# Kernel optimization log

Measured on AMD Instinct MI355X. Metric: run time of the kernel, lower is better.

## Reference

```python
import math
import jax, jax.numpy as jnp
import numpy as np


def conv2d(x, w, stride=1, padding=0, groups=1):
    return jax.lax.conv_general_dilated(
        x, w, (stride, stride), [(padding, padding), (padding, padding)],
        feature_group_count=groups, dimension_numbers=('NCHW', 'OIHW', 'NCHW'))


def bn_relu(x, g, b, eps=1e-5):
    # training-mode batchnorm (batch statistics, biased var) + ReLU
    m = x.mean(axis=(0, 2, 3), keepdims=True)
    v = x.var(axis=(0, 2, 3), keepdims=True)
    y = (x - m) * jax.lax.rsqrt(v + eps)
    return jax.nn.relu(y * g[None, :, None, None] + b[None, :, None, None])


def up2x(x):
    B, C, H, W = x.shape
    return jax.image.resize(x, (B, C, 2 * H, 2 * W), 'bilinear')


def pos2d(C, H, W):
    # faithful port of ReasonDecoder.pos2d -> [H*W, 1, C]
    dm = C // 2
    div = jnp.exp(jnp.arange(0.0, dm, 2.0) * (-(math.log(10000.0) / dm)))  # [dm//2]
    pos_w = jnp.arange(0.0, W)[:, None]
    pos_h = jnp.arange(0.0, H)[:, None]
    sw = jnp.sin(pos_w * div).T  # [dm//2, W]
    cw = jnp.cos(pos_w * div).T
    sh = jnp.sin(pos_h * div).T  # [dm//2, H]
    ch = jnp.cos(pos_h * div).T
    pe = jnp.zeros((C, H, W))
    pe = pe.at[0:dm:2].set(jnp.broadcast_to(sw[:, None, :], (dm // 2, H, W)))
    pe = pe.at[1:dm:2].set(jnp.broadcast_to(cw[:, None, :], (dm // 2, H, W)))
    pe = pe.at[dm::2].set(jnp.broadcast_to(sh[:, :, None], (dm // 2, H, W)))
    pe = pe.at[dm + 1::2].set(jnp.broadcast_to(ch[:, :, None], (dm // 2, H, W)))
    return pe.reshape(C, 1, H * W).transpose(2, 1, 0)


def setup_inputs() -> dict:
    key = jax.random.key(0)
    ks = jax.random.split(key, 32)
    B, C, H, W = 8, 512, 32, 32
    Cv = 256  # in_dim of Projector
    KS = 3
    s = 0.02
    inp = {
        'image_embeddings': jax.random.normal(ks[0], (B, C, H, W), jnp.float32),
        'sparse_prompt_embeddings': jax.random.normal(ks[1], (B, 2, C), jnp.float32),
        'state': jax.random.normal(ks[2], (B, C), jnp.float32),
        'multimask_output': 0,
        # stand-in transformer: single linear on (src + pos)
        'W_t': jax.random.normal(ks[3], (C, C), jnp.float32) * s,
        'iou_token': jax.random.normal(ks[4], (1, C), jnp.float32) * s,
        'mask_tokens': jax.random.normal(ks[5], (4, C), jnp.float32) * s,
        # Projector.vis
        'vis_conv1_w': jax.random.normal(ks[6], (2 * Cv, 2 * Cv, 3, 3), jnp.float32) * s,
        'vis_bn1_g': jnp.ones((2 * Cv,), jnp.float32),
        'vis_bn1_b': jnp.zeros((2 * Cv,), jnp.float32),
        'vis_conv2_w': jax.random.normal(ks[7], (Cv, 2 * Cv, 3, 3), jnp.float32) * s,
        'vis_bn2_g': jnp.ones((Cv,), jnp.float32),
        'vis_bn2_b': jnp.zeros((Cv,), jnp.float32),
        'vis_conv3_w': jax.random.normal(ks[8], (Cv, Cv, 1, 1), jnp.float32) * s,
        'vis_conv3_b': jnp.zeros((Cv,), jnp.float32),
        # Projector.txt -> Linear(512, 256*3*3 + 1)
        'txt_w': jax.random.normal(ks[9], (Cv * KS * KS + 1, C), jnp.float32) * s,
        'txt_b': jnp.zeros((Cv * KS * KS + 1,), jnp.float32),
        # 1x1 convs as linears
        'ln_ans_w': jax.random.normal(ks[10], (512, 512), jnp.float32) * s,
        'ln_ans_b': jnp.zeros((512,), jnp.float32),
        'ln_ans2_w': jax.random.normal(ks[11], (128, 512), jnp.float32) * s,
        'ln_ans2_b': jnp.zeros((128,), jnp.float32),
        # router: Linear(1024,256) -> ReLU -> Linear(256,8)
        'router_w1': jax.random.normal(ks[12], (256, 1024), jnp.float32) * s,
        'router_b1': jnp.zeros((256,), jnp.float32),
        'router_w2': jax.random.normal(ks[13], (8, 256), jnp.float32) * s,
        'router_b2': jnp.zeros((8,), jnp.float32),
        # 8 experts: Linear(128, 23) each, stacked
        'experts_w': jax.random.normal(ks[14], (8, 23, 128), jnp.float32) * s,
        'experts_b': jnp.zeros((8, 23), jnp.float32),
    }
    return inp


def reference(image_embeddings, sparse_prompt_embeddings, state, multimask_output,
              W_t, iou_token, mask_tokens,
              vis_conv1_w, vis_bn1_g, vis_bn1_b,
              vis_conv2_w, vis_bn2_g, vis_bn2_b,
              vis_conv3_w, vis_conv3_b,
              txt_w, txt_b, ln_ans_w, ln_ans_b, ln_ans2_w, ln_ans2_b,
              router_w1, router_b1, router_w2, router_b2,
              experts_w, experts_b):
    B, C, H, W = image_embeddings.shape
    pe = pos2d(C, H, W)  # [HW,1,C]

    # tokens = [iou, mask tokens, sparse prompts] (passed to transformer; hs unused)
    out_tok = jnp.concatenate([iou_token, mask_tokens], axis=0)  # [5,C]
    tokens = jnp.concatenate(
        [jnp.broadcast_to(out_tok[None], (B,) + out_tok.shape), sparse_prompt_embeddings], axis=1)
    del tokens  # hs is discarded by predict_masks

    # stand-in transformer: src_out = Linear(src_flat + pos)
    src_flat = image_embeddings.reshape(B, C, H * W).transpose(0, 2, 1) + pe[:, 0, :][None]  # [B,HW,C]
    src_flat = jnp.einsum('bnc,dc->bnd', src_flat, W_t)
    src = src_flat.transpose(0, 2, 1).reshape(B, C, H, W)

    # ---- Projector ----
    ans = src.mean(axis=(2, 3))                              # global avg pool [B,512]
    ans_vec = ans @ ln_ans_w.T + ln_ans_b                    # 1x1 conv [B,512]

    x = up2x(src)
    x = bn_relu(conv2d(x, vis_conv1_w, padding=1), vis_bn1_g, vis_bn1_b)
    x = up2x(x)
    x = bn_relu(conv2d(x, vis_conv2_w, padding=1), vis_bn2_g, vis_bn2_b)
    x = conv2d(x, vis_conv3_w) + vis_conv3_b[None, :, None, None]  # [B,256,4H,4W]
    Bx, Cx, Hx, Wx = x.shape

    qa = jnp.concatenate([state, ans_vec], axis=1)           # [B,1024]
    o = jax.nn.softmax(qa, axis=1) * qa
    half = o.shape[1] // 2
    word = o[:, :half] + o[:, half:]                         # [B,512]
    word = word @ txt_w.T + txt_b                            # [B, 256*9+1]
    dyn_w = word[:, :-1].reshape(B, Cx, 3, 3)                # per-sample conv weights
    dyn_b = word[:, -1]                                      # [B]

    xg = x.reshape(1, B * Cx, Hx, Wx)
    out = conv2d(xg, dyn_w, padding=1, groups=B) + dyn_b[None, :, None, None]  # [1,B,Hx,Wx]
    masks = out.transpose(1, 0, 2, 3)                        # [B,1,Hx,Wx]

    gates = jax.nn.softmax(
        jax.nn.relu(qa @ router_w1.T + router_b1) @ router_w2.T + router_b2, axis=1)  # [B,8]
    feat128 = ans_vec @ ln_ans2_w.T + ln_ans2_b              # [B,128]
    logits = jnp.einsum('be,eof,bf->bo', gates, experts_w, feat128) + gates @ experts_b  # [B,23]

    masks = masks[:, 1:, :, :] if multimask_output else masks[:, 0:1, :, :]
    return masks, logits, src
```

## Files before the change

kernel.cpp:

```cpp
#include <hip/hip_runtime.h>
#include <hip/hip_bf16.h>

typedef __attribute__((ext_vector_type(8))) short short8;
typedef __attribute__((ext_vector_type(4))) short shortx4;
typedef __attribute__((ext_vector_type(4))) float floatx4;
typedef __attribute__((ext_vector_type(16))) float floatx16;

#define F2BF __float2bfloat16
#define BF2F __bfloat162float

#define WS_W4R2   0UL
#define WS_WRO2   9437184UL
#define WS_WRO1   11796480UL
#define WS_Y1     16515072UL
#define WS_Y2     50069504UL
#define WS_W4R1   50069504UL
#define WS_A      68943872UL
#define WS_WTB    77332480UL
#define WS_SRCB   77856768UL
#define WS_STATS  117178368UL
#define WS_ANS    117186560UL
#define WS_QA     117207040UL
#define WS_ANSV   117239808UL
#define WS_WORD   117256192UL
#define WS_WORD2  117272576UL
#define WS_EFFW   117346336UL
#define WS_EFFB   117420064UL
#define WS_HID    117420352UL

#define OUT_LOGITS 131072
#define OUT_SRC    131256

__device__ __forceinline__ float inp(const void* p, long i, int isbf) {
    return isbf ? BF2F(((const __hip_bfloat16*)p)[i]) : ((const float*)p)[i];
}
__device__ __forceinline__ void outw(void* p, long i, float v, int isbf) {
    if (isbf) ((__hip_bfloat16*)p)[i] = F2BF(v);
    else      ((float*)p)[i] = v;
}
__device__ __forceinline__ float bfbits2f(short s) {
    unsigned int u = ((unsigned int)(unsigned short)s) << 16;
    float f; __builtin_memcpy(&f, &u, 4); return f;
}
__device__ __forceinline__ short f2bfbits(float f) {
    __hip_bfloat16 h = F2BF(f);
    short s; __builtin_memcpy(&s, &h, 2); return s;
}

__device__ __forceinline__ int detect_bf(const void* img) {
    const unsigned short* u = (const unsigned short*)img;
    int l = threadIdx.x & 63;
    int c = 0;
#pragma unroll
    for (int k = 0; k < 8; ++k) {
        int e = (u[(l * 8 + k) * 2] >> 7) & 0xFF;
        c += (e >= 100 && e <= 150) ? 1 : 0;
    }
    for (int off = 32; off; off >>= 1) c += __shfl_xor(c, off, 64);
    return c > 307;
}

__device__ __forceinline__ float pe_val(int n, int c) {
    float pos = (c < 256) ? (float)(n & 31) : (float)(n >> 5);
    int i = ((c < 256) ? c : (c - 256)) >> 1;
    float ang = pos * expf(-0.0719557841560639f * (float)i);
    return (c & 1) ? cosf(ang) : sinf(ang);
}

__global__ void k_pre(const void* __restrict__ img, const void* __restrict__ cw1,
                      const void* __restrict__ cw2, const void* __restrict__ Wt,
                      __hip_bfloat16* __restrict__ A,
                      __hip_bfloat16* __restrict__ W4R1, __hip_bfloat16* __restrict__ W4R2,
                      __hip_bfloat16* __restrict__ WRo1, __hip_bfloat16* __restrict__ WRo2,
                      __hip_bfloat16* __restrict__ WTB) {
    int isbf = detect_bf(img);
    int bid = blockIdx.x, tid = threadIdx.x;
    __shared__ float LS[2304];
    if (bid < 4096) {
        int nt = bid & 31, ct = (bid >> 5) & 15, b = bid >> 9;
        int tx = tid & 31, ty = tid >> 5;
        int c0 = ct * 32, n0 = nt * 32;
        for (int j = 0; j < 4; ++j) {
            int c = c0 + ty + j * 8;
            LS[(ty + j * 8) * 33 + tx] = inp(img, ((long)(b * 512 + c)) * 1024 + n0 + tx, isbf);
        }
        __syncthreads();
        for (int j = 0; j < 4; ++j) {
            int n = n0 + ty + j * 8, c = c0 + tx;
            A[((long)(b * 1024 + n)) * 512 + c] = F2BF(LS[tx * 33 + ty + j * 8] + pe_val(n, c));
        }
    } else if (bid < 5632) {
        int bb = bid - 4096;
        const void* w; __hip_bfloat16 *w4, *wo; int Cout, r0;
        if (bb < 1024) { w = cw1; w4 = W4R1; wo = WRo1; Cout = 512; r0 = bb * 256; }
        else           { w = cw2; w4 = W4R2; wo = WRo2; Cout = 256; r0 = (bb - 1024) * 256; }
        int Cout4 = Cout << 2;
        int G = Cout4 >> 5;
        int co = r0 >> 9, ci0 = r0 & 511;
        for (int e = tid; e < 2304; e += 256) LS[e] = inp(w, (long)r0 * 9 + e, isbf);
        __syncthreads();
        int ci = ci0 + tid;
        int cc = ci >> 5, cw = ci & 31;
        int ksub = (ci >> 4) & 1, hic = (ci >> 3) & 1, ee = ci & 7;
        float w9[9];
#pragma unroll
        for (int t = 0; t < 9; ++t) w9[t] = LS[tid * 9 + t];
#pragma unroll
        for (int t = 0; t < 9; ++t)
            wo[((long)(t * 16 + cc) * Cout + co) * 32 + cw] = F2BF(w9[t]);
        const float BY[2][3][3] = {{{0.75f, 0.25f, 0.f}, {0.25f, 0.75f, 0.75f}, {0.f, 0.f, 0.25f}},
                                   {{0.25f, 0.f, 0.f},  {0.75f, 0.75f, 0.25f}, {0.f, 0.25f, 0.75f}}};
#pragma unroll
        for (int p = 0; p < 4; ++p) {
            int py = p >> 1, px = p & 1;
            int co4 = p * Cout + co;
            int cog = co4 >> 5, l31c = co4 & 31;
#pragma unroll
            for (int dy = 0; dy < 3; ++dy)
#pragma unroll
            for (int dx = 0; dx < 3; ++dx) {
                float v = 0.f;
#pragma unroll
                for (int ky = 0; ky < 3; ++ky)
#pragma unroll
                for (int kx = 0; kx < 3; ++kx)
                    v += BY[py][dy][ky] * BY[px][dx][kx] * w9[ky * 3 + kx];
                long fi = ((((long)((dy * 3 + dx) * 16 + cc) * G + cog) * 2 + ksub) * 64
                           + hic * 32 + l31c) * 8 + ee;
                w4[fi] = F2BF(v);
            }
        }
    } else {
        for (int i = (bid - 5632) * 256 + tid; i < 512 * 512; i += 256 * 256)
            WTB[i] = F2BF(inp(Wt, i, isbf));
    }
}

__global__ __launch_bounds__(256) void k_gemm1(const __hip_bfloat16* __restrict__ A,
                                               const __hip_bfloat16* __restrict__ Bw,
                                               __hip_bfloat16* __restrict__ srcB,
                                               void* __restrict__ dst,
                                               float* __restrict__ ANS,
                                               const void* __restrict__ img) {
    int isbf = detect_bf(img);
    __shared__ __align__(16) __hip_bfloat16 As[128 * 32];
    __shared__ __align__(16) __hip_bfloat16 Bs[128 * 32];
    int m0 = blockIdx.x * 128, n0 = blockIdx.y * 128;
    int tid = threadIdx.x;
    int wave = tid >> 6, l = tid & 63, lm = l & 15, q = l >> 4;
    int wm = wave & 1, wn = wave >> 1;
    int m_0 = tid >> 2, qq0 = tid & 3;
    int m_1 = (tid + 256) >> 2, qq1 = qq0;
    const __hip_bfloat16* aA0 = A + ((long)(m0 + m_0)) * 512 + qq0 * 8;
    const __hip_bfloat16* aB0 = Bw + ((long)(n0 + m_0)) * 512 + qq0 * 8;
    const __hip_bfloat16* aA1 = A + ((long)(m0 + m_1)) * 512 + qq1 * 8;
    const __hip_bfloat16* aB1 = Bw + ((long)(n0 + m_1)) * 512 + qq1 * 8;
    int wA0 = m_0 * 32 + qq0 * 8, wA1 = m_1 * 32 + qq1 * 8;
    short8 rA0 = *(const short8*)(aA0), rB0 = *(const short8*)(aB0);
    short8 rA1 = *(const short8*)(aA1), rB1 = *(const short8*)(aB1);
    floatx4 zero4 = {0.f, 0.f, 0.f, 0.f};
    floatx4 acc[4][4];
    for (int i = 0; i < 4; ++i) for (int j = 0; j < 4; ++j) acc[i][j] = zero4;
    for (int k0 = 0; k0 < 512; k0 += 32) {
        __syncthreads();
        *(short8*)(As + wA0) = rA0; *(short8*)(Bs + wA0) = rB0;
        *(short8*)(As + wA1) = rA1; *(short8*)(Bs + wA1) = rB1;
        __syncthreads();
        if (k0 < 480) {
            rA0 = *(const short8*)(aA0 + k0 + 32); rB0 = *(const short8*)(aB0 + k0 + 32);
            rA1 = *(const short8*)(aA1 + k0 + 32); rB1 = *(const short8*)(aB1 + k0 + 32);
        }
        short8 af[4], bfv[4];
#pragma unroll
        for (int t = 0; t < 4; ++t) af[t] = *(short8*)(As + (wm * 64 + t * 16 + lm) * 32 + q * 8);
#pragma unroll
        for (int t = 0; t < 4; ++t) bfv[t] = *(short8*)(Bs + (wn * 64 + t * 16 + lm) * 32 + q * 8);
#pragma unroll
        for (int i = 0; i < 4; ++i)
#pragma unroll
            for (int j = 0; j < 4; ++j)
                acc[i][j] = __builtin_amdgcn_mfma_f32_16x16x32_bf16(af[i], bfv[j], acc[i][j], 0, 0, 0);
    }
    int b = m0 >> 10, hw0 = m0 & 1023;
    float cs[4] = {0.f, 0.f, 0.f, 0.f};
#pragma unroll
    for (int i = 0; i < 4; ++i)
#pragma unroll
        for (int j = 0; j < 4; ++j) {
            int mrow = wm * 64 + i * 16 + q * 4;
            int n = n0 + wn * 64 + j * 16 + lm;
            long mg = (long)(m0 + mrow);
#pragma unroll
            for (int r = 0; r < 4; ++r) {
                float v = acc[i][j][r];
                srcB[(mg + r) * 512 + n] = F2BF(v);
                cs[j] += v;
            }
            long obase = (long)OUT_SRC + ((long)(b * 512 + n)) * 1024 + hw0 + mrow;
            if (isbf) {
                shortx4 pk = { f2bfbits(acc[i][j][0]), f2bfbits(acc[i][j][1]),
                               f2bfbits(acc[i][j][2]), f2bfbits(acc[i][j][3]) };
                *(shortx4*)((__hip_bfloat16*)dst + obase) = pk;
            } else {
                floatx4 pk = { acc[i][j][0], acc[i][j][1], acc[i][j][2], acc[i][j][3] };
                *(floatx4*)((float*)dst + obase) = pk;
            }
        }
#pragma unroll
    for (int j = 0; j < 4; ++j) {
        cs[j] += __shfl_xor(cs[j], 16);
        cs[j] += __shfl_xor(cs[j], 32);
    }
    __syncthreads();
    float* CS = (float*)Bs;
    if (wm == 1 && q == 0) {
#pragma unroll
        for (int j = 0; j < 4; ++j) CS[wn * 64 + j * 16 + lm] = cs[j];
    }
    __syncthreads();
    if (wm == 0 && q == 0) {
#pragma unroll
        for (int j = 0; j < 4; ++j) {
            int n = n0 + wn * 64 + j * 16 + lm;
            atomicAdd(ANS + b * 512 + n, cs[j] + CS[wn * 64 + j * 16 + lm]);
        }
    }
}

__global__ void k_ansvec(const float* __restrict__ ANS, const void* __restrict__ lw,
                         const void* __restrict__ lb, float* __restrict__ ansv,
                         const void* __restrict__ img) {
    int isbf = detect_bf(img);
    int b = blockIdx.x, dt = blockIdx.y, tid = threadIdx.x;
    __shared__ float aL[512];
    __shared__ float R[256];
    aL[tid] = ANS[b * 512 + tid] * (1.f / 1024.f);
    aL[tid + 256] = ANS[b * 512 + tid + 256] * (1.f / 1024.f);
    __syncthreads();
    int d = dt * 64 + (tid >> 2), cl = tid & 3;
    float acc = 0.f;
    for (int k = 0; k < 128; ++k) {
        int c = cl + 4 * k;
        acc += aL[c] * inp(lw, (long)d * 512 + c, isbf);
    }
    R[tid] = acc;
    __syncthreads();
    if (cl == 0)
        ansv[b * 512 + d] = R[tid] + R[tid + 1] + R[tid + 2] + R[tid + 3] + inp(lb, d, isbf);
}

__global__ void k_word(const float* __restrict__ ansv, const void* __restrict__ state,
                       float* __restrict__ qa, float* __restrict__ word,
                       const void* __restrict__ img) {
    int isbf = detect_bf(img);
    int b = blockIdx.x, tid = threadIdx.x;
    __shared__ float L[1024];
    __shared__ float red[256];
    L[tid] = inp(state, b * 512 + tid, isbf);
    L[tid + 256] = inp(state, b * 512 + tid + 256, isbf);
    L[tid + 512] = ansv[b * 512 + tid];
    L[tid + 768] = ansv[b * 512 + tid + 256];
    __syncthreads();
    for (int j = tid; j < 1024; j += 256) qa[b * 1024 + j] = L[j];
    float m = fmaxf(fmaxf(L[tid], L[tid + 256]), fmaxf(L[tid + 512], L[tid + 768]));
    red[tid] = m; __syncthreads();
    for (int s = 128; s > 0; s >>= 1) { if (tid < s) red[tid] = fmaxf(red[tid], red[tid + s]); __syncthreads(); }
    float M = red[0]; __syncthreads();
    float z = expf(L[tid] - M) + expf(L[tid + 256] - M) + expf(L[tid + 512] - M) + expf(L[tid + 768] - M);
    red[tid] = z; __syncthreads();
    for (int s = 128; s > 0; s >>= 1) { if (tid < s) red[tid] += red[tid + s]; __syncthreads(); }
    float Z = red[0];
    for (int j = tid; j < 512; j += 256) {
        float o1 = expf(L[j] - M) / Z * L[j];
        float o2 = expf(L[j + 512] - M) / Z * L[j + 512];
        word[b * 512 + j] = o1 + o2;
    }
}

__global__ void k_txt(const float* __restrict__ word, const void* __restrict__ tw,
                      const void* __restrict__ tb, float* __restrict__ word2,
                      const void* __restrict__ img) {
    int isbf = detect_bf(img);
    int n = blockIdx.x, tid = threadIdx.x;
    __shared__ float wL[8][512];
    __shared__ float red[256 * 8];
    for (int e = tid; e < 4096; e += 256) wL[e >> 9][e & 511] = word[e];
    __syncthreads();
    float acc[8] = {0, 0, 0, 0, 0, 0, 0, 0};
    for (int c = tid; c < 512; c += 256) {
        float tv = inp(tw, (long)n * 512 + c, isbf);
        for (int b = 0; b < 8; ++b) acc[b] += wL[b][c] * tv;
    }
    for (int b = 0; b < 8; ++b) red[tid * 8 + b] = acc[b];
    __syncthreads();
    for (int s = 128; s > 0; s >>= 1) {
        if (tid < s) for (int b = 0; b < 8; ++b) red[tid * 8 + b] += red[(tid + s) * 8 + b];
        __syncthreads();
    }
    if (tid < 8) word2[tid * 2305 + n] = red[tid] + inp(tb, n, isbf);
}

__global__ void k_eff(const float* __restrict__ word2, const void* __restrict__ w3,
                      const void* __restrict__ b3, float* __restrict__ effw,
                      float* __restrict__ effb, const void* __restrict__ img) {
    int isbf = detect_bf(img);
    int bid = blockIdx.x;
    int b = bid / 9, tap = bid - b * 9;
    int tid = threadIdx.x;
    __shared__ float dw[256];
    dw[tid] = word2[b * 2305 + tid * 9 + tap];
    __syncthreads();
    float acc = 0.f;
    for (int c = 0; c < 256; ++c) acc += dw[c] * inp(w3, c * 256 + tid, isbf);
    effw[(b * 9 + tap) * 256 + tid] = acc;
    if (tid == 0) {
        float e = 0.f;
        for (int c = 0; c < 256; ++c) e += dw[c] * inp(b3, c, isbf);
        effb[b * 9 + tap] = e;
    }
}

__device__ __forceinline__ void epi32(const floatx16& Acc, int pxbase, int co4,
        int csh, int Cout, int tY, int tX, int b, int OW2, int hi,
        __hip_bfloat16* __restrict__ out, float& s1, float& s2) {
    int par = co4 >> csh; int co = co4 & (Cout - 1);
    int fyo = par >> 1, fxo = par & 1;
#pragma unroll
    for (int r = 0; r < 16; ++r) {
        int row = (r & 3) + 8 * (r >> 2) + 4 * hi;
        int px = pxbase + row;
        int fy = (((tY << 3) + (px >> 4)) << 1) + fyo;
        int fx = (((tX << 4) + (px & 15)) << 1) + fxo;
        float v = Acc[r];
        out[(((long)(b * OW2 + fy)) * OW2 + fx) * Cout + co] = F2BF(v);
        s1 += v; s2 += v * v;
    }
}

__global__ __launch_bounds__(256, 3) void k_conv4(const __hip_bfloat16* __restrict__ in,
        const __hip_bfloat16* __restrict__ w4, __hip_bfloat16* __restrict__ out,
        int inH, int inW, int Cout, float* __restrict__ s1o, float* __restrict__ s2o,
        const float* __restrict__ bnS1, const float* __restrict__ bnS2,
        const void* __restrict__ g, const void* __restrict__ bb, float invN,
        const void* __restrict__ img) {
    int Cout4 = Cout << 2;
    int csh = (Cout == 512) ? 9 : 8;
    int G = Cout4 >> 5;
    int tXn = inW >> 4, tYn = inH >> 3;
    int bid = blockIdx.y;
    int tX = bid % tXn; int tmp = bid / tXn; int tY = tmp % tYn; int b = tmp / tYn;
    int co0 = blockIdx.x * 128;
    __shared__ __align__(16) __hip_bfloat16 Hs[4 * 180 * 8];
    __shared__ float scT[512], shT[512];
    int tid = threadIdx.x;
    int l = tid & 63, l31 = l & 31, hi = l >> 5;
    int wave = tid >> 6;
    int wm = wave & 1, wn = wave >> 1;
    int dobn = (bnS1 != nullptr);
    if (dobn) {
        int isbf = detect_bf(img);
        for (int c = tid; c < 512; c += 256) {
            float m = bnS1[c] * invN, var = bnS2[c] * invN - m * m;
            float sc = inp(g, c, isbf) * rsqrtf(var + 1e-5f);
            scT[c] = sc; shT[c] = inp(bb, c, isbf) - m * sc;
        }
    }
    int R0 = (tY << 3) - 1, C0 = (tX << 4) - 1;
    long base = (long)b * inH * inW;
    int sub = tid & 3;
    const __hip_bfloat16* ga[3];
    int wo[3];
#pragma unroll
    for (int s = 0; s < 3; ++s) {
        int gi = tid + s * 256;
        int p = gi >> 2; if (p > 179) p = 179;
        int hy = p / 18, hx = p - hy * 18;
        int gr = R0 + hy; gr = gr < 0 ? 0 : (gr > inH - 1 ? inH - 1 : gr);
        int gc = C0 + hx; gc = gc < 0 ? 0 : (gc > inW - 1 ? inW - 1 : gc);
        ga[s] = in + (base + (long)gr * inW + gc) * 512 + sub * 8;
        wo[s] = (sub * 180 + p) * 8;
    }
    int has2 = (tid < 208);
    short8 r0 = *(const short8*)(ga[0]);
    short8 r1 = *(const short8*)(ga[1]);
    short8 r2 = {0, 0, 0, 0, 0, 0, 0, 0};
    if (has2) r2 = *(const short8*)(ga[2]);
    int qA = hi * 1440;
    int qB = qA + 2880;
    int h0, h1;
    {
        int px0 = wm * 64 + l31;
        int px1 = px0 + 32;
        h0 = ((px0 >> 4) * 18 + (px0 & 15)) * 8;
        h1 = ((px1 >> 4) * 18 + (px1 & 15)) * 8;
    }
    const __hip_bfloat16* wl2 = w4 + (long)l * 8;
    int cg0 = (co0 >> 5) + wn * 2;
    short8 wS0[4], wS1[4], wS2[4];
#define LDW(S, t, c) { long fb = (((long)((t) * 16 + (c)) * G + cg0) * 2) * 512; \
    S[0] = *(const short8*)(wl2 + fb);             \
    S[1] = *(const short8*)(wl2 + fb + 512);       \
    S[2] = *(const short8*)(wl2 + fb + 1024);      \
    S[3] = *(const short8*)(wl2 + fb + 1536); }
    floatx16 zero16 = {0,0,0,0,0,0,0,0,0,0,0,0,0,0,0,0};
    floatx16 a00 = zero16, a01 = zero16, a10 = zero16, a11 = zero16;
    LDW(wS0, 0, 0);
    for (int ci0 = 0; ci0 < 512; ci0 += 32) {
        int cc = ci0 >> 5;
        __syncthreads();
        if (dobn) {
            float scv[8], shv[8];
#pragma unroll
            for (int k = 0; k < 8; ++k) { int c = ci0 + sub * 8 + k; scv[k] = scT[c]; shv[k] = shT[c]; }
#pragma unroll
            for (int k = 0; k < 8; ++k) {
                float f0 = bfbits2f(r0[k]) * scv[k] + shv[k]; r0[k] = f2bfbits(f0 > 0.f ? f0 : 0.f);
                float f1 = bfbits2f(r1[k]) * scv[k] + shv[k]; r1[k] = f2bfbits(f1 > 0.f ? f1 : 0.f);
                float f2 = bfbits2f(r2[k]) * scv[k] + shv[k]; r2[k] = f2bfbits(f2 > 0.f ? f2 : 0.f);
            }
        }
        *(short8*)(Hs + wo[0]) = r0;
        *(short8*)(Hs + wo[1]) = r1;
        if (has2) *(short8*)(Hs + wo[2]) = r2;
        __syncthreads();
        if (ci0 < 480) {
            r0 = *(const short8*)(ga[0] + ci0 + 32);
            r1 = *(const short8*)(ga[1] + ci0 + 32);
            if (has2) r2 = *(const short8*)(ga[2] + ci0 + 32);
        }
#pragma unroll
        for (int tap = 0; tap < 9; ++tap) {
            {
                int nt = tap + 1, ncc = cc;
                if (nt == 9) { nt = 0; ncc = cc + 1; }
                if (ncc < 16) {
                    if (((tap + 1) % 3) == 0)      { LDW(wS0, nt, ncc); }
                    else if (((tap + 1) % 3) == 1) { LDW(wS1, nt, ncc); }
                    else                            { LDW(wS2, nt, ncc); }
                }
            }
            int dy = tap / 3, dx = tap - dy * 3;
            int hoE = (dy * 18 + dx) * 8;
            short8 af00 = *(const short8*)(Hs + qA + h0 + hoE);
            short8 af01 = *(const short8*)(Hs + qB + h0 + hoE);
            short8 af10 = *(const short8*)(Hs + qA + h1 + hoE);
            short8 af11 = *(const short8*)(Hs + qB + h1 + hoE);
            if ((tap % 3) == 0) {
                a00 = __builtin_amdgcn_mfma_f32_32x32x16_bf16(af00, wS0[0], a00, 0, 0, 0);
                a00 = __builtin_amdgcn_mfma_f32_32x32x16_bf16(af01, wS0[1], a00, 0, 0, 0);
                a01 = __builtin_amdgcn_mfma_f32_32x32x16_bf16(af00, wS0[2], a01, 0, 0, 0);
                a01 = __builtin_amdgcn_mfma_f32_32x32x16_bf16(af01, wS0[3], a01, 0, 0, 0);
                a10 = __builtin_amdgcn_mfma_f32_32x32x16_bf16(af10, wS0[0], a10, 0, 0, 0);
                a10 = __builtin_amdgcn_mfma_f32_32x32x16_bf16(af11, wS0[1], a10, 0, 0, 0);
                a11 = __builtin_amdgcn_mfma_f32_32x32x16_bf16(af10, wS0[2], a11, 0, 0, 0);
                a11 = __builtin_amdgcn_mfma_f32_32x32x16_bf16(af11, wS0[3], a11, 0, 0, 0);
            } else if ((tap % 3) == 1) {
                a00 = __builtin_amdgcn_mfma_f32_32x32x16_bf16(af00, wS1[0], a00, 0, 0, 0);
                a00 = __builtin_amdgcn_mfma_f32_32x32x16_bf16(af01, wS1[1], a00, 0, 0, 0);
                a01 = __builtin_amdgcn_mfma_f32_32x32x16_bf16(af00, wS1[2], a01, 0, 0, 0);
                a01 = __builtin_amdgcn_mfma_f32_32x32x16_bf16(af01, wS1[3], a01, 0, 0, 0);
                a10 = __builtin_amdgcn_mfma_f32_32x32x16_bf16(af10, wS1[0], a10, 0, 0, 0);
                a10 = __builtin_amdgcn_mfma_f32_32x32x16_bf16(af11, wS1[1], a10, 0, 0, 0);
                a11 = __builtin_amdgcn_mfma_f32_32x32x16_bf16(af10, wS1[2], a11, 0, 0, 0);
                a11 = __builtin_amdgcn_mfma_f32_32x32x16_bf16(af11, wS1[3], a11, 0, 0, 0);
            } else {
                a00 = __builtin_amdgcn_mfma_f32_32x32x16_bf16(af00, wS2[0], a00, 0, 0, 0);
                a00 = __builtin_amdgcn_mfma_f32_32x32x16_bf16(af01, wS2[1], a00, 0, 0, 0);
                a01 = __builtin_amdgcn_mfma_f32_32x32x16_bf16(af00, wS2[2], a01, 0, 0, 0);
                a01 = __builtin_amdgcn_mfma_f32_32x32x16_bf16(af01, wS2[3], a01, 0, 0, 0);
                a10 = __builtin_amdgcn_mfma_f32_32x32x16_bf16(af10, wS2[0], a10, 0, 0, 0);
                a10 = __builtin_amdgcn_mfma_f32_32x32x16_bf16(af11, wS2[1], a10, 0, 0, 0);
                a11 = __builtin_amdgcn_mfma_f32_32x32x16_bf16(af10, wS2[2], a11, 0, 0, 0);
                a11 = __builtin_amdgcn_mfma_f32_32x32x16_bf16(af11, wS2[3], a11, 0, 0, 0);
            }
        }
    }
#undef LDW
    int OW2 = inW << 1;
    float s1v0 = 0.f, s2v0 = 0.f, s1v1 = 0.f, s2v1 = 0.f;
    {
        int pxb0 = wm * 64, pxb1 = wm * 64 + 32;
        int co4a = co0 + wn * 64 + l31;
        int co4b = co4a + 32;
        epi32(a00, pxb0, co4a, csh, Cout, tY, tX, b, OW2, hi, out, s1v0, s2v0);
        epi32(a10, pxb1, co4a, csh, Cout, tY, tX, b, OW2, hi, out, s1v0, s2v0);
        epi32(a01, pxb0, co4b, csh, Cout, tY, tX, b, OW2, hi, out, s1v1, s2v1);
        epi32(a11, pxb1, co4b, csh, Cout, tY, tX, b, OW2, hi, out, s1v1, s2v1);
    }
    s1v0 += __shfl_xor(s1v0, 32); s2v0 += __shfl_xor(s2v0, 32);
    s1v1 += __shfl_xor(s1v1, 32); s2v1 += __shfl_xor(s2v1, 32);
    __syncthreads();
    float* RB = (float*)Hs;
    if (wm == 1 && hi == 0) {
        int i0 = wn * 64 + l31, i1 = i0 + 32;
        RB[i0] = s1v0; RB[128 + i0] = s2v0;
        RB[i1] = s1v1; RB[128 + i1] = s2v1;
    }
    __syncthreads();
    if (wm == 0 && hi == 0) {
        int i0 = wn * 64 + l31, i1 = i0 + 32;
        atomicAdd(s1o + ((co0 + i0) & (Cout - 1)), s1v0 + RB[i0]);
        atomicAdd(s2o + ((co0 + i0) & (Cout - 1)), s2v0 + RB[128 + i0]);
        atomicAdd(s1o + ((co0 + i1) & (Cout - 1)), s1v1 + RB[i1]);
        atomicAdd(s2o + ((co0 + i1) & (Cout - 1)), s2v1 + RB[128 + i1]);
    }
}

__global__ __launch_bounds__(256) void k_efix(const __hip_bfloat16* __restrict__ in,
        __hip_bfloat16* __restrict__ Y, const __hip_bfloat16* __restrict__ wRo,
        int inW, int Cout, int ebase,
        float* __restrict__ s1o, float* __restrict__ s2o) {
    int OW = inW << 1;
    int coT = Cout >> 6;
    int b = blockIdx.x / coT, cot = blockIdx.x - b * coT;
    int co0 = cot << 6;
    int e = ebase + blockIdx.y;
    __shared__ __align__(16) __hip_bfloat16 E[130 * 40];
    __shared__ __align__(16) __hip_bfloat16 Lline[64 * 32];
    int tid = threadIdx.x;
    int wave = tid >> 6, l = tid & 63, lm = l & 15, q = l >> 4;
    int mspan = OW >> 2;
    int ilim = OW >> 6;
    int mb = wave * mspan;
    floatx4 zero4 = {0.f, 0.f, 0.f, 0.f};
    floatx4 acc[2][4];
    for (int i = 0; i < 2; ++i) for (int j = 0; j < 4; ++j) acc[i][j] = zero4;
    int lineG = inW * 4;
    int eG = (OW + 2) * 4;
    int haveL = (tid < lineG);
    const __hip_bfloat16* lbase = in;
    {
        int x = tid >> 2, sb = tid & 3;
        long gidx;
        if (e < 2) { int R = (e == 0) ? 0 : inW - 1; gidx = (long)(b * inW + R) * inW + x; }
        else       { int Cc = (e == 2) ? 0 : inW - 1; gidx = (long)(b * inW + x) * inW + Cc; }
        if (x >= inW) gidx = (long)b * inW * inW;
        lbase = in + gidx * 512 + sb * 8;
    }
    short8 rl = {0, 0, 0, 0, 0, 0, 0, 0};
    if (haveL) rl = *(const short8*)(lbase);
    for (int ci0 = 0; ci0 < 512; ci0 += 32) {
        __syncthreads();
        if (haveL) *(short8*)(Lline + tid * 8) = rl;
        __syncthreads();
        if (ci0 < 480 && haveL) rl = *(const short8*)(lbase + ci0 + 32);
        for (int t = tid; t < eG; t += 256) {
            int f1 = t >> 2, sb = t & 3;
            int f = f1 - 1;
            short8 res = {0, 0, 0, 0, 0, 0, 0, 0};
            if (f < 0 || f >= OW) {
                if (e < 2) { int xx = (f < 0) ? 0 : inW - 1; res = *(const short8*)(Lline + (xx * 4 + sb) * 8); }
            } else {
                int x0; float w0;
                if (f & 1) { x0 = f >> 1; w0 = 0.75f; } else { x0 = (f >> 1) - 1; w0 = 0.25f; }
                int x1 = x0 + 1;
                if (x0 < 0) x0 = 0;
                if (x1 > inW - 1) x1 = inW - 1;
                short8 v0 = *(const short8*)(Lline + (x0 * 4 + sb) * 8);
                short8 v1 = *(const short8*)(Lline + (x1 * 4 + sb) * 8);
                float w1c = 1.f - w0;
#pragma unroll
                for (int k = 0; k < 8; ++k)
                    res[k] = f2bfbits(w0 * bfbits2f(v0[k]) + w1c * bfbits2f(v1[k]));
            }
            *(short8*)(E + f1 * 40 + sb * 8) = res;
        }
        __syncthreads();
        int cc = ci0 >> 5;
#pragma unroll
        for (int t = 0; t < 3; ++t) {
            int tap = (e == 0) ? t : (e == 1) ? (6 + t) : (e == 2) ? (t * 3) : (t * 3 + 2);
            short8 bfv[4];
#pragma unroll
            for (int j = 0; j < 4; ++j)
                bfv[j] = *(const short8*)(wRo + ((long)(tap * 16 + cc) * Cout + co0 + j * 16 + lm) * 32 + q * 8);
#pragma unroll
            for (int i = 0; i < 2; ++i) {
                if (i < ilim) {
                    short8 af = *(const short8*)(E + (mb + i * 16 + lm + t) * 40 + q * 8);
#pragma unroll
                    for (int j = 0; j < 4; ++j)
                        acc[i][j] = __builtin_amdgcn_mfma_f32_16x16x32_bf16(af, bfv[j], acc[i][j], 0, 0, 0);
                }
            }
        }
    }
    float d1s[4] = {0.f, 0.f, 0.f, 0.f}, d2s[4] = {0.f, 0.f, 0.f, 0.f};
    for (int i = 0; i < ilim; ++i)
#pragma unroll
    for (int j = 0; j < 4; ++j) {
        int co = co0 + j * 16 + lm;
#pragma unroll
        for (int r = 0; r < 4; ++r) {
            int m = mb + i * 16 + q * 4 + r;
            int fy, fx;
            if (e == 0) { fy = 0; fx = m; }
            else if (e == 1) { fy = OW - 1; fx = m; }
            else if (e == 2) { fy = m; fx = 0; }
            else { fy = m; fx = OW - 1; }
            long a = (((long)(b * OW + fy)) * OW + fx) * Cout + co;
            float vo = BF2F(Y[a]);
            float vn = vo - acc[i][j][r];
            Y[a] = F2BF(vn);
            d1s[j] += vn - vo;
            d2s[j] += vn * vn - vo * vo;
        }
    }
#pragma unroll
    for (int j = 0; j < 4; ++j) {
        d1s[j] += __shfl_xor(d1s[j], 16); d1s[j] += __shfl_xor(d1s[j], 32);
        d2s[j] += __shfl_xor(d2s[j], 16); d2s[j] += __shfl_xor(d2s[j], 32);
    }
    if (q == 0) {
#pragma unroll
        for (int j = 0; j < 4; ++j) {
            atomicAdd(s1o + co0 + j * 16 + lm, d1s[j]);
            atomicAdd(s2o + co0 + j * 16 + lm, d2s[j]);
        }
    }
}

__global__ __launch_bounds__(256) void k_masks(const __hip_bfloat16* __restrict__ x2,
                                               const float* __restrict__ effw,
                                               const float* __restrict__ effb,
                                               const float* __restrict__ word2,
                                               void* __restrict__ mout,
                                               const float* __restrict__ s1,
                                               const float* __restrict__ s2,
                                               const void* __restrict__ g,
                                               const void* __restrict__ bb, float invN,
                                               const void* __restrict__ img) {
    int isbf = detect_bf(img);
    int bid = blockIdx.x;
    int tX = bid & 15, tY = (bid >> 4) & 15, b = bid >> 8;
    __shared__ __align__(16) __hip_bfloat16 H[100 * 264];
    __shared__ __align__(16) float EW[9 * 256];
    __shared__ float EB[9];
    __shared__ float sc2T[256];
    __shared__ float sh2T[256];
    int tid = threadIdx.x;
    {
        float m = s1[tid] * invN, var = s2[tid] * invN - m * m;
        float sc = inp(g, tid, isbf) * rsqrtf(var + 1e-5f);
        sc2T[tid] = sc; sh2T[tid] = inp(bb, tid, isbf) - m * sc;
    }
    __syncthreads();
    for (int e = tid; e < 3200; e += 256) {
        int c8 = e & 31, p = e >> 5;
        int hy = p / 10, hx = p - hy * 10;
        int gy = tY * 8 + hy - 1, gx = tX * 8 + hx - 1;
        short8 res = {0, 0, 0, 0, 0, 0, 0, 0};
        if (gy >= 0 && gy < 128 && gx >= 0 && gx < 128) {
            short8 raw = *(const short8*)(x2 + (((long)(b * 128 + gy)) * 128 + gx) * 256 + c8 * 8);
#pragma unroll
            for (int k = 0; k < 8; ++k) {
                int c = c8 * 8 + k;
                float v = bfbits2f(raw[k]) * sc2T[c] + sh2T[c];
                res[k] = f2bfbits(v > 0.f ? v : 0.f);
            }
        }
        *(short8*)(H + p * 264 + c8 * 8) = res;
    }
    for (int e = tid; e < 2304; e += 256) EW[e] = effw[b * 2304 + e];
    if (tid < 9) EB[tid] = effb[b * 9 + tid];
    __syncthreads();
    int px = tid & 63, part = tid >> 6;
    int py = px >> 3, pxc = px & 7;
    int cbase = part * 64;
    float acc = 0.f;
    for (int tap = 0; tap < 9; ++tap) {
        int ky = tap / 3, kx = tap - ky * 3;
        int hp = (py + ky) * 10 + pxc + kx;
        const __hip_bfloat16* hrow = H + (long)hp * 264 + cbase;
        const float* erow = EW + tap * 256 + cbase;
#pragma unroll
        for (int c8 = 0; c8 < 8; ++c8) {
            short8 h8 = *(const short8*)(hrow + c8 * 8);
            floatx4 e0 = *(const floatx4*)(erow + c8 * 8);
            floatx4 e1 = *(const floatx4*)(erow + c8 * 8 + 4);
            acc += bfbits2f(h8[0]) * e0[0] + bfbits2f(h8[1]) * e0[1] +
                   bfbits2f(h8[2]) * e0[2] + bfbits2f(h8[3]) * e0[3] +
                   bfbits2f(h8[4]) * e1[0] + bfbits2f(h8[5]) * e1[1] +
                   bfbits2f(h8[6]) * e1[2] + bfbits2f(h8[7]) * e1[3];
        }
    }
    float (*red)[64] = (float(*)[64])sc2T;
    red[part][px] = acc;
    __syncthreads();
    if (part == 0) {
        float s = red[0][px] + red[1][px] + red[2][px] + red[3][px];
        int oy = tY * 8 + py, ox = tX * 8 + pxc;
        float bias = word2[b * 2305 + 2304];
        for (int tap = 0; tap < 9; ++tap) {
            int ky = tap / 3, kx = tap - ky * 3;
            int iy = oy + ky - 1, ix = ox + kx - 1;
            if (iy >= 0 && iy < 128 && ix >= 0 && ix < 128) bias += EB[tap];
        }
        outw(mout, b * 16384 + oy * 128 + ox, s + bias, isbf);
    }
}

__global__ void k_hid(const float* __restrict__ qa, const void* __restrict__ w1,
                      const void* __restrict__ b1, float* __restrict__ hid,
                      const void* __restrict__ img) {
    int isbf = detect_bf(img);
    int b = blockIdx.x, ht = blockIdx.y, tid = threadIdx.x;
    __shared__ float qL[1024];
    __shared__ float R[256];
    for (int j = tid; j < 1024; j += 256) qL[j] = qa[b * 1024 + j];
    __syncthreads();
    int h = ht * 64 + (tid >> 2), cl = tid & 3;
    float acc = 0.f;
    for (int k = 0; k < 256; ++k) {
        int c = cl + 4 * k;
        acc += qL[c] * inp(w1, (long)h * 1024 + c, isbf);
    }
    R[tid] = acc;
    __syncthreads();
    if (cl == 0) {
        float v = R[tid] + R[tid + 1] + R[tid + 2] + R[tid + 3] + inp(b1, h, isbf);
        hid[b * 256 + h] = v > 0.f ? v : 0.f;
    }
}

__global__ void k_logits(const float* __restrict__ hid, const float* __restrict__ ansv,
                         const void* __restrict__ w2, const void* __restrict__ b2,
                         const void* __restrict__ lw2, const void* __restrict__ lb2,
                         const void* __restrict__ ew, const void* __restrict__ ebias,
                         void* __restrict__ out, const void* __restrict__ img) {
    int isbf = detect_bf(img);
    int b = blockIdx.x, tid = threadIdx.x;
    __shared__ float hidL[256], avL[512], gates[8], feat[128], R[256];
    hidL[tid] = hid[b * 256 + tid];
    for (int j = tid; j < 512; j += 256) avL[j] = ansv[b * 512 + j];
    __syncthreads();
    if (tid < 8) {
        float gl = inp(b2, tid, isbf);
        for (int j = 0; j < 256; ++j) gl += hidL[j] * inp(w2, tid * 256 + j, isbf);
        gates[tid] = gl;
    }
    int f = tid >> 1, half = tid & 1;
    float acc = 0.f;
    for (int k = 0; k < 256; ++k) {
        int c = half + 2 * k;
        acc += avL[c] * inp(lw2, (long)f * 512 + c, isbf);
    }
    R[tid] = acc;
    __syncthreads();
    if (tid == 0) {
        float mx = gates[0];
        for (int e = 1; e < 8; ++e) mx = fmaxf(mx, gates[e]);
        float z = 0.f;
        for (int e = 0; e < 8; ++e) { gates[e] = expf(gates[e] - mx); z += gates[e]; }
        for (int e = 0; e < 8; ++e) gates[e] /= z;
    }
    if (half == 0) feat[f] = R[tid] + R[tid + 1] + inp(lb2, f, isbf);
    __syncthreads();
    if (tid < 23) {
        float a = 0.f;
        for (int e = 0; e < 8; ++e) {
            float d = inp(ebias, e * 23 + tid, isbf);
            for (int ff = 0; ff < 128; ++ff) d += inp(ew, (e * 23 + tid) * 128 + ff, isbf) * feat[ff];
            a += gates[e] * d;
        }
        outw(out, OUT_LOGITS + b * 23 + tid, a, isbf);
    }
}

extern "C" void kernel_launch(void* const* d_in, const int* in_sizes, int n_in,
                              void* d_out, int out_size, void* d_ws, size_t ws_size,
                              hipStream_t stream) {
    (void)in_sizes; (void)n_in; (void)out_size; (void)ws_size;
    const void* img   = d_in[0];
    const void* state = d_in[2];
    const void* Wt    = d_in[4];
    const void* cw1   = d_in[7];
    const void* g1    = d_in[8];
    const void* bb1   = d_in[9];
    const void* cw2   = d_in[10];
    const void* g2    = d_in[11];
    const void* bb2   = d_in[12];
    const void* w3    = d_in[13];
    const void* b3    = d_in[14];
    const void* txtw  = d_in[15];
    const void* txtb  = d_in[16];
    const void* lnw   = d_in[17];
    const void* lnb   = d_in[18];
    const void* lnw2  = d_in[19];
    const void* lnb2  = d_in[20];
    const void* rw1   = d_in[21];
    const void* rb1   = d_in[22];
    const void* rw2   = d_in[23];
    const void* rb2   = d_in[24];
    const void* ew    = d_in[25];
    const void* eb    = d_in[26];

    char* ws = (char*)d_ws;
    __hip_bfloat16* W4R2 = (__hip_bfloat16*)(ws + WS_W4R2);
    __hip_bfloat16* WRO2 = (__hip_bfloat16*)(ws + WS_WRO2);
    __hip_bfloat16* WRO1 = (__hip_bfloat16*)(ws + WS_WRO1);
    __hip_bfloat16* Y1   = (__hip_bfloat16*)(ws + WS_Y1);
    __hip_bfloat16* Y2   = (__hip_bfloat16*)(ws + WS_Y2);
    __hip_bfloat16* W4R1 = (__hip_bfloat16*)(ws + WS_W4R1);
    __hip_bfloat16* A    = (__hip_bfloat16*)(ws + WS_A);
    __hip_bfloat16* WTB  = (__hip_bfloat16*)(ws + WS_WTB);
    __hip_bfloat16* SRCB = (__hip_bfloat16*)(ws + WS_SRCB);
    float* S1A = (float*)(ws + WS_STATS);
    float* S2A = S1A + 512;
    float* S1B = S1A + 1024;
    float* S2B = S1A + 1536;
    float* ANS   = (float*)(ws + WS_ANS);
    float* QA    = (float*)(ws + WS_QA);
    float* ANSV  = (float*)(ws + WS_ANSV);
    float* WORD  = (float*)(ws + WS_WORD);
    float* WORD2 = (float*)(ws + WS_WORD2);
    float* EFFW  = (float*)(ws + WS_EFFW);
    float* EFFB  = (float*)(ws + WS_EFFB);
    float* HID   = (float*)(ws + WS_HID);

    hipMemsetAsync(ws + WS_STATS, 0, 24576, stream);

    k_pre<<<5888, 256, 0, stream>>>(img, cw1, cw2, Wt, A, W4R1, W4R2, WRO1, WRO2, WTB);
    k_gemm1<<<dim3(64, 4), 256, 0, stream>>>(A, WTB, SRCB, d_out, ANS, img);
    k_ansvec<<<dim3(8, 8), 256, 0, stream>>>(ANS, lnw, lnb, ANSV, img);
    k_word<<<8, 256, 0, stream>>>(ANSV, state, QA, WORD, img);
    k_txt<<<2305, 256, 0, stream>>>(WORD, txtw, txtb, WORD2, img);
    k_eff<<<72, 256, 0, stream>>>(WORD2, w3, b3, EFFW, EFFB, img);
    k_conv4<<<dim3(16, 64), 256, 0, stream>>>(SRCB, W4R1, Y1, 32, 32, 512, S1A, S2A,
                                              nullptr, nullptr, nullptr, nullptr, 0.f, img);
    k_efix<<<dim3(64, 2), 256, 0, stream>>>(SRCB, Y1, WRO1, 32, 512, 0, S1A, S2A);
    k_efix<<<dim3(64, 2), 256, 0, stream>>>(SRCB, Y1, WRO1, 32, 512, 2, S1A, S2A);
    k_conv4<<<dim3(8, 256), 256, 0, stream>>>(Y1, W4R2, Y2, 64, 64, 256, S1B, S2B,
                                              S1A, S2A, g1, bb1, 1.f / 32768.f, img);
    k_efix<<<dim3(32, 2), 256, 0, stream>>>(Y1, Y2, WRO2, 64, 256, 0, S1B, S2B);
    k_efix<<<dim3(32, 2), 256, 0, stream>>>(Y1, Y2, WRO2, 64, 256, 2, S1B, S2B);
    k_masks<<<2048, 256, 0, stream>>>(Y2, EFFW, EFFB, WORD2, d_out,
                                      S1B, S2B, g2, bb2, 1.f / 131072.f, img);
    k_hid<<<dim3(8, 4), 256, 0, stream>>>(QA, rw1, rb1, HID, img);
    k_logits<<<8, 256, 0, stream>>>(HID, ANSV, rw2, rb2, lnw2, lnb2, ew, eb, d_out, img);
}
```

Before: 1.042 ms.

## Remap conv4 waves to 128px x 32co tiles and pad LDS halo stride

The per-wave tile of the conv4 MFMA kernel changes from 64 pixels x 64 output channels (2x2 grid of waves) to 128 pixels x 32 channels (one channel group per wave). Each wave now loads half as many weight registers from global memory but reads twice as many A fragments from LDS. The LDS sub-plane stride is padded from 1440 to 1448 elements, presumably to reduce bank conflicts. Because each wave already covers every pixel, the cross-wave shared-memory reduction of batch-norm statistics and its two barriers are dropped, and each wave issues its own atomics.

```diff
diff --git a/kernel.cpp b/kernel.cpp
--- a/kernel.cpp
+++ b/kernel.cpp
@@ -350,12 +350,11 @@
     int bid = blockIdx.y;
     int tX = bid % tXn; int tmp = bid / tXn; int tY = tmp % tYn; int b = tmp / tYn;
     int co0 = blockIdx.x * 128;
-    __shared__ __align__(16) __hip_bfloat16 Hs[4 * 180 * 8];
+    __shared__ __align__(16) __hip_bfloat16 Hs[4 * 1448];
     __shared__ float scT[512], shT[512];
     int tid = threadIdx.x;
     int l = tid & 63, l31 = l & 31, hi = l >> 5;
     int wave = tid >> 6;
-    int wm = wave & 1, wn = wave >> 1;
     int dobn = (bnS1 != nullptr);
     if (dobn) {
         int isbf = detect_bf(img);
@@ -378,32 +377,31 @@
         int gr = R0 + hy; gr = gr < 0 ? 0 : (gr > inH - 1 ? inH - 1 : gr);
         int gc = C0 + hx; gc = gc < 0 ? 0 : (gc > inW - 1 ? inW - 1 : gc);
         ga[s] = in + (base + (long)gr * inW + gc) * 512 + sub * 8;
-        wo[s] = (sub * 180 + p) * 8;
+        wo[s] = sub * 1448 + p * 8;
     }
     int has2 = (tid < 208);
     short8 r0 = *(const short8*)(ga[0]);
     short8 r1 = *(const short8*)(ga[1]);
     short8 r2 = {0, 0, 0, 0, 0, 0, 0, 0};
     if (has2) r2 = *(const short8*)(ga[2]);
-    int qA = hi * 1440;
-    int qB = qA + 2880;
-    int h0, h1;
-    {
-        int px0 = wm * 64 + l31;
-        int px1 = px0 + 32;
-        h0 = ((px0 >> 4) * 18 + (px0 & 15)) * 8;
-        h1 = ((px1 >> 4) * 18 + (px1 & 15)) * 8;
+    int qA = hi * 1448;
+    int qB = qA + 2896;
+    int h[4];
+#pragma unroll
+    for (int i = 0; i < 4; ++i) {
+        int px = i * 32 + l31;
+        h[i] = ((px >> 4) * 18 + (px & 15)) * 8;
     }
     const __hip_bfloat16* wl2 = w4 + (long)l * 8;
-    int cg0 = (co0 >> 5) + wn * 2;
-    short8 wS0[4], wS1[4], wS2[4];
-#define LDW(S, t, c) { long fb = (((long)((t) * 16 + (c)) * G + cg0) * 2) * 512; \
+    int cgw = (co0 >> 5) + wave;
+    short8 wS0[2], wS1[2], wS2[2];
+#define LDW(S, t, c) { long fb = (((long)((t) * 16 + (c)) * G + cgw) * 2) * 512; \
     S[0] = *(const short8*)(wl2 + fb);             \
-    S[1] = *(const short8*)(wl2 + fb + 512);       \
-    S[2] = *(const short8*)(wl2 + fb + 1024);      \
-    S[3] = *(const short8*)(wl2 + fb + 1536); }
+    S[1] = *(const short8*)(wl2 + fb + 512); }
     floatx16 zero16 = {0,0,0,0,0,0,0,0,0,0,0,0,0,0,0,0};
-    floatx16 a00 = zero16, a01 = zero16, a10 = zero16, a11 = zero16;
+    floatx16 a[4];
+#pragma unroll
+    for (int i = 0; i < 4; ++i) a[i] = zero16;
     LDW(wS0, 0, 0);
     for (int ci0 = 0; ci0 < 512; ci0 += 32) {
         int cc = ci0 >> 5;
@@ -441,68 +439,45 @@
             }
             int dy = tap / 3, dx = tap - dy * 3;
             int hoE = (dy * 18 + dx) * 8;
-            short8 af00 = *(const short8*)(Hs + qA + h0 + hoE);
-            short8 af01 = *(const short8*)(Hs + qB + h0 + hoE);
-            short8 af10 = *(const short8*)(Hs + qA + h1 + hoE);
-            short8 af11 = *(const short8*)(Hs + qB + h1 + hoE);
             if ((tap % 3) == 0) {
-                a00 = __builtin_amdgcn_mfma_f32_32x32x16_bf16(af00, wS0[0], a00, 0, 0, 0);
-                a00 = __builtin_amdgcn_mfma_f32_32x32x16_bf16(af01, wS0[1], a00, 0, 0, 0);
-                a01 = __builtin_amdgcn_mfma_f32_32x32x16_bf16(af00, wS0[2], a01, 0, 0, 0);
-                a01 = __builtin_amdgcn_mfma_f32_32x32x16_bf16(af01, wS0[3], a01, 0, 0, 0);
-                a10 = __builtin_amdgcn_mfma_f32_32x32x16_bf16(af10, wS0[0], a10, 0, 0, 0);
-                a10 = __builtin_amdgcn_mfma_f32_32x32x16_bf16(af11, wS0[1], a10, 0, 0, 0);
-                a11 = __builtin_amdgcn_mfma_f32_32x32x16_bf16(af10, wS0[2], a11, 0, 0, 0);
-                a11 = __builtin_amdgcn_mfma_f32_32x32x16_bf16(af11, wS0[3], a11, 0, 0, 0);
+#pragma unroll
+                for (int i = 0; i < 4; ++i) {
+                    short8 af0 = *(const short8*)(Hs + qA + h[i] + hoE);
+                    short8 af1 = *(const short8*)(Hs + qB + h[i] + hoE);
+                    a[i] = __builtin_amdgcn_mfma_f32_32x32x16_bf16(af0, wS0[0], a[i], 0, 0, 0);
+                    a[i] = __builtin_amdgcn_mfma_f32_32x32x16_bf16(af1, wS0[1], a[i], 0, 0, 0);
+                }
             } else if ((tap % 3) == 1) {
-                a00 = __builtin_amdgcn_mfma_f32_32x32x16_bf16(af00, wS1[0], a00, 0, 0, 0);
-                a00 = __builtin_amdgcn_mfma_f32_32x32x16_bf16(af01, wS1[1], a00, 0, 0, 0);
-                a01 = __builtin_amdgcn_mfma_f32_32x32x16_bf16(af00, wS1[2], a01, 0, 0, 0);
-                a01 = __builtin_amdgcn_mfma_f32_32x32x16_bf16(af01, wS1[3], a01, 0, 0, 0);
-                a10 = __builtin_amdgcn_mfma_f32_32x32x16_bf16(af10, wS1[0], a10, 0, 0, 0);
-                a10 = __builtin_amdgcn_mfma_f32_32x32x16_bf16(af11, wS1[1], a10, 0, 0, 0);
-                a11 = __builtin_amdgcn_mfma_f32_32x32x16_bf16(af10, wS1[2], a11, 0, 0, 0);
-                a11 = __builtin_amdgcn_mfma_f32_32x32x16_bf16(af11, wS1[3], a11, 0, 0, 0);
+#pragma unroll
+                for (int i = 0; i < 4; ++i) {
+                    short8 af0 = *(const short8*)(Hs + qA + h[i] + hoE);
+                    short8 af1 = *(const short8*)(Hs + qB + h[i] + hoE);
+                    a[i] = __builtin_amdgcn_mfma_f32_32x32x16_bf16(af0, wS1[0], a[i], 0, 0, 0);
+                    a[i] = __builtin_amdgcn_mfma_f32_32x32x16_bf16(af1, wS1[1], a[i], 0, 0, 0);
+                }
             } else {
-                a00 = __builtin_amdgcn_mfma_f32_32x32x16_bf16(af00, wS2[0], a00, 0, 0, 0);
-                a00 = __builtin_amdgcn_mfma_f32_32x32x16_bf16(af01, wS2[1], a00, 0, 0, 0);
-                a01 = __builtin_amdgcn_mfma_f32_32x32x16_bf16(af00, wS2[2], a01, 0, 0, 0);
-                a01 = __builtin_amdgcn_mfma_f32_32x32x16_bf16(af01, wS2[3], a01, 0, 0, 0);
-                a10 = __builtin_amdgcn_mfma_f32_32x32x16_bf16(af10, wS2[0], a10, 0, 0, 0);
-                a10 = __builtin_amdgcn_mfma_f32_32x32x16_bf16(af11, wS2[1], a10, 0, 0, 0);
-                a11 = __builtin_amdgcn_mfma_f32_32x32x16_bf16(af10, wS2[2], a11, 0, 0, 0);
-                a11 = __builtin_amdgcn_mfma_f32_32x32x16_bf16(af11, wS2[3], a11, 0, 0, 0);
+#pragma unroll
+                for (int i = 0; i < 4; ++i) {
+                    short8 af0 = *(const short8*)(Hs + qA + h[i] + hoE);
+                    short8 af1 = *(const short8*)(Hs + qB + h[i] + hoE);
+                    a[i] = __builtin_amdgcn_mfma_f32_32x32x16_bf16(af0, wS2[0], a[i], 0, 0, 0);
+                    a[i] = __builtin_amdgcn_mfma_f32_32x32x16_bf16(af1, wS2[1], a[i], 0, 0, 0);
+                }
             }
         }
     }
 #undef LDW
     int OW2 = inW << 1;
-    float s1v0 = 0.f, s2v0 = 0.f, s1v1 = 0.f, s2v1 = 0.f;
-    {
-        int pxb0 = wm * 64, pxb1 = wm * 64 + 32;
-        int co4a = co0 + wn * 64 + l31;
-        int co4b = co4a + 32;
-        epi32(a00, pxb0, co4a, csh, Cout, tY, tX, b, OW2, hi, out, s1v0, s2v0);
-        epi32(a10, pxb1, co4a, csh, Cout, tY, tX, b, OW2, hi, out, s1v0, s2v0);
-        epi32(a01, pxb0, co4b, csh, Cout, tY, tX, b, OW2, hi, out, s1v1, s2v1);
-        epi32(a11, pxb1, co4b, csh, Cout, tY, tX, b, OW2, hi, out, s1v1, s2v1);
-    }
-    s1v0 += __shfl_xor(s1v0, 32); s2v0 += __shfl_xor(s2v0, 32);
-    s1v1 += __shfl_xor(s1v1, 32); s2v1 += __shfl_xor(s2v1, 32);
-    __syncthreads();
-    float* RB = (float*)Hs;
-    if (wm == 1 && hi == 0) {
-        int i0 = wn * 64 + l31, i1 = i0 + 32;
-        RB[i0] = s1v0; RB[128 + i0] = s2v0;
-        RB[i1] = s1v1; RB[128 + i1] = s2v1;
-    }
-    __syncthreads();
-    if (wm == 0 && hi == 0) {
-        int i0 = wn * 64 + l31, i1 = i0 + 32;
-        atomicAdd(s1o + ((co0 + i0) & (Cout - 1)), s1v0 + RB[i0]);
-        atomicAdd(s2o + ((co0 + i0) & (Cout - 1)), s2v0 + RB[128 + i0]);
-        atomicAdd(s1o + ((co0 + i1) & (Cout - 1)), s1v1 + RB[i1]);
-        atomicAdd(s2o + ((co0 + i1) & (Cout - 1)), s2v1 + RB[128 + i1]);
+    float s1v = 0.f, s2v = 0.f;
+    int co4w = co0 + wave * 32 + l31;
+#pragma unroll
+    for (int i = 0; i < 4; ++i)
+        epi32(a[i], i * 32, co4w, csh, Cout, tY, tX, b, OW2, hi, out, s1v, s2v);
+    s1v += __shfl_xor(s1v, 32); s2v += __shfl_xor(s2v, 32);
+    if (hi == 0) {
+        int ch = co4w & (Cout - 1);
+        atomicAdd(s1o + ch, s1v);
+        atomicAdd(s2o + ch, s2v);
     }
 }
 
```

After: 1.045 ms. No clear change (+0.3%).
